# Optimization experiments

Measured on AMD Instinct MI355X. Metric: run time of the kernel, lower is better.

The kernel has to match this reference:

```python
import jax, jax.numpy as jnp
import numpy as np

B, L, D = 4, 2048, 1024

def setup_inputs() -> dict:
    key = jax.random.key(0)
    k = jax.random.split(key, 5)
    s = 1.0 / np.sqrt(D)
    return {
        "x": jax.random.normal(k[0], (B, L, D), dtype=jnp.float32),
        "W1": jax.random.uniform(k[1], (D, D), jnp.float32, -s, s),
        "b1": jax.random.uniform(k[2], (D,), jnp.float32, -s, s),
        "W2": jax.random.uniform(k[3], (D, D), jnp.float32, -s, s),
        "b2": jax.random.uniform(k[4], (D,), jnp.float32, -s, s),
    }

def reference(x, W1, b1, W2, b2):
    # query = fc1(x), value = fc2(x); torch Linear: x @ W^T + b
    query = jnp.einsum("bld,ed->ble", x, W1) + b1   # [B,L,D]
    value = jnp.einsum("bld,ed->ble", x, W2) + b2   # [B,L,D]
    # attn = softmax(query @ value^T)  (dot attention, no scaling in original)
    scores = jnp.einsum("bqd,bkd->bqk", query, value)  # [B,L,L]
    attn = jax.nn.softmax(scores, axis=-1)
    # dropout_p=0.0 -> identity
    return jnp.einsum("bqk,bkd->bqd", attn, value)     # [B,L,D]
```

## Files before the change

kernel.cpp:

```cpp
#include <hip/hip_runtime.h>
#include <stdint.h>
#include <stddef.h>


typedef _Float16  f16_t;
typedef _Float16  f16x8 __attribute__((ext_vector_type(8)));
typedef float     f32x4 __attribute__((ext_vector_type(4)));

__device__ __forceinline__ f32x4 mfma16(f16x8 a, f16x8 b, f32x4 c) {
  return __builtin_amdgcn_mfma_f32_16x16x32_f16(a, b, c, 0, 0, 0);
}

__device__ __forceinline__ void async_copy16(const f16_t* g, f16_t* l) {
  __builtin_amdgcn_global_load_lds(
      (const __attribute__((address_space(1))) unsigned int*)(g),
      (__attribute__((address_space(3))) unsigned int*)(l),
      16, 0, 0);
}

template <int RM, int RN, int NS>
__device__ __forceinline__ void gemm_core(
    const f16_t* __restrict__ A, const f16_t* __restrict__ B,
    int lda, int ldb, int nk,
    f16_t* __restrict__ As, f16_t* __restrict__ Bs, f32x4 (&acc)[RM][RN])
{
  const int tid  = threadIdx.x;
  const int lane = tid & 63;
  const int w    = tid >> 6;
  const int wr   = (w >> 1) * (RM * 16);
  const int wc   = (w & 1) * (RN * 16);
  const int l16  = lane & 15;
  const int quad = lane >> 4;
  const int sw   = (quad ^ ((l16 >> 1) & 3)) * 8;

  const int r0  = tid >> 2;
  const int kc0 = ((tid & 3) ^ ((r0 >> 1) & 3)) * 8;

  const f16_t* Ag = A + (size_t)r0 * lda + kc0;
  const f16_t* Bg = B + (size_t)r0 * ldb + kc0;

  for (int kt = 0; kt < nk; ++kt) {
#pragma unroll
    for (int s = 0; s < NS; ++s) {
      const int ko = s * 32;
#pragma unroll
      for (int h = 0; h < RM / 2; ++h)
        async_copy16(Ag + ko + (size_t)(64 * h) * lda,
                     As + s * RM * 1024 + (tid + 256 * h) * 8);
#pragma unroll
      for (int h = 0; h < RN / 2; ++h)
        async_copy16(Bg + ko + (size_t)(64 * h) * ldb,
                     Bs + s * RN * 1024 + (tid + 256 * h) * 8);
    }
    __syncthreads();

#pragma unroll
    for (int s = 0; s < NS; ++s) {
      const f16_t* Ac = As + s * RM * 1024;
      const f16_t* Bc = Bs + s * RN * 1024;
      f16x8 af[RM], bf[RN];
#pragma unroll
      for (int i = 0; i < RM; ++i)
        af[i] = *(const f16x8*)(Ac + (wr + i * 16 + l16) * 32 + sw);
#pragma unroll
      for (int j = 0; j < RN; ++j)
        bf[j] = *(const f16x8*)(Bc + (wc + j * 16 + l16) * 32 + sw);
#pragma unroll
      for (int i = 0; i < RM; ++i)
#pragma unroll
        for (int j = 0; j < RN; ++j)
          acc[i][j] = mfma16(af[i], bf[j], acc[i][j]);
    }

    __syncthreads();
    Ag += NS * 32; Bg += NS * 32;
  }
}

__global__ __launch_bounds__(256) void cvt_kernel(
    const float* __restrict__ x, const float* __restrict__ W1,
    const float* __restrict__ W2, f16_t* __restrict__ xh,
    f16_t* __restrict__ W1h, f16_t* __restrict__ W2h)
{
  const size_t XN = (size_t)8192 * 1024;
  const size_t WN = (size_t)1024 * 1024;
  size_t i = ((size_t)blockIdx.x * 256 + threadIdx.x) * 8;
  const float* in; f16_t* out;
  if (i < XN)            { in = x;  out = xh; }
  else if (i < XN + WN)  { in = W1; out = W1h; i -= XN; }
  else                   { in = W2; out = W2h; i -= XN + WN; }
  f32x4 a = *(const f32x4*)(in + i);
  f32x4 b = *(const f32x4*)(in + i + 4);
  f16x8 o;
#pragma unroll
  for (int k = 0; k < 4; ++k) { o[k] = (f16_t)a[k]; o[k + 4] = (f16_t)b[k]; }
  *(f16x8*)(out + i) = o;
}

__global__ __launch_bounds__(256) void proj_qv_kernel(
    const f16_t* __restrict__ X, const f16_t* __restrict__ W1,
    const f16_t* __restrict__ W2, const float* __restrict__ b1,
    const float* __restrict__ b2, f16_t* __restrict__ Q,
    f16_t* __restrict__ V)
{
  __shared__ __align__(16) f16_t Xs[2 * 64 * 32];
  __shared__ __align__(16) f16_t W1s[2 * 64 * 32];
  __shared__ __align__(16) f16_t W2s[2 * 64 * 32];
  constexpr int SZ = 64 * 32;

  const int m0 = blockIdx.x * 64;
  const int n0 = blockIdx.y * 64;

  const int tid  = threadIdx.x;
  const int lane = tid & 63;
  const int w    = tid >> 6;
  const int wr   = (w >> 1) * 32;
  const int wc   = (w & 1) * 32;
  const int quad = lane >> 4;
  const int l16  = lane & 15;
  const int sw   = (quad ^ ((l16 >> 1) & 3)) * 8;
  const int r0   = tid >> 2;
  const int kc0  = ((tid & 3) ^ ((r0 >> 1) & 3)) * 8;

  const f16_t* Xg = X + (size_t)(m0 + r0) * 1024 + kc0;
  const f16_t* G1 = W1 + (size_t)(n0 + r0) * 1024 + kc0;
  const f16_t* G2 = W2 + (size_t)(n0 + r0) * 1024 + kc0;

  f32x4 accQ[2][2] = {};
  f32x4 accV[2][2] = {};

  for (int kt = 0; kt < 16; ++kt) {
#pragma unroll
    for (int s = 0; s < 2; ++s) {
      const int ko = s * 32;
      async_copy16(Xg + ko, Xs + s * SZ + tid * 8);
      async_copy16(G1 + ko, W1s + s * SZ + tid * 8);
      async_copy16(G2 + ko, W2s + s * SZ + tid * 8);
    }
    __syncthreads();

#pragma unroll
    for (int s = 0; s < 2; ++s) {
      f16x8 xf[2], w1f[2], w2f[2];
#pragma unroll
      for (int i = 0; i < 2; ++i) {
        xf[i]  = *(const f16x8*)(Xs  + s * SZ + (wr + i * 16 + l16) * 32 + sw);
        w1f[i] = *(const f16x8*)(W1s + s * SZ + (wc + i * 16 + l16) * 32 + sw);
        w2f[i] = *(const f16x8*)(W2s + s * SZ + (wc + i * 16 + l16) * 32 + sw);
      }
#pragma unroll
      for (int i = 0; i < 2; ++i)
#pragma unroll
        for (int j = 0; j < 2; ++j) {
          accQ[i][j] = mfma16(xf[i], w1f[j], accQ[i][j]);
          accV[i][j] = mfma16(xf[i], w2f[j], accV[i][j]);
        }
    }
    __syncthreads();
    Xg += 64; G1 += 64; G2 += 64;
  }

#pragma unroll
  for (int j = 0; j < 2; ++j) {
    const int col = n0 + wc + j * 16 + l16;
    const float bq = b1[col], bv = b2[col];
#pragma unroll
    for (int i = 0; i < 2; ++i)
#pragma unroll
      for (int r = 0; r < 4; ++r) {
        const int row = m0 + wr + i * 16 + quad * 4 + r;
        Q[(size_t)row * 1024 + col] = (f16_t)(accQ[i][j][r] + bq);
        V[(size_t)row * 1024 + col] = (f16_t)(accV[i][j][r] + bv);
      }
  }
}

__global__ __launch_bounds__(256) void vt_kernel(
    const f16_t* __restrict__ V, f16_t* __restrict__ Vt)
{
  __shared__ __align__(16) f16_t Ls[64 * 64];
  const int key0 = blockIdx.x * 64;
  const int d0   = blockIdx.y * 64;
  const size_t boff = (size_t)blockIdx.z * 2048 * 1024;

  const int tid = threadIdx.x;
#pragma unroll
  for (int rep = 0; rep < 2; ++rep) {
    const int kr = rep * 32 + (tid >> 3);
    const int dc = (tid & 7) * 8;
    f16x8 v = *(const f16x8*)(V + boff + (size_t)(key0 + kr) * 1024 + d0 + dc);
#pragma unroll
    for (int e = 0; e < 8; ++e) {
      const int d = dc + e;
      Ls[d * 64 + (((kr >> 3) ^ (d >> 3)) << 3) + (kr & 7)] = v[e];
    }
  }
  __syncthreads();
#pragma unroll
  for (int rep = 0; rep < 2; ++rep) {
    const int d = rep * 32 + (tid >> 3);
    const int c = tid & 7;
    f16x8 v = *(const f16x8*)(Ls + d * 64 + ((c ^ (d >> 3)) << 3));
    *(f16x8*)(Vt + boff + (size_t)(d0 + d) * 2048 + key0 + c * 8) = v;
  }
}

__global__ __launch_bounds__(256) void score_kernel(
    const f16_t* __restrict__ Q, const f16_t* __restrict__ V,
    f16_t* __restrict__ S)
{
  __shared__ __align__(16) f16_t As[2 * 128 * 32];
  __shared__ __align__(16) f16_t Bs[2 * 128 * 32];
  const int m0 = blockIdx.x * 128;
  const int n0 = blockIdx.y * 128;
  const size_t boff = (size_t)blockIdx.z * 2048 * 1024;

  f32x4 acc[4][4] = {};
  gemm_core<4, 4, 2>(Q + boff + (size_t)m0 * 1024,
                     V + boff + (size_t)n0 * 1024,
                     1024, 1024, 1024 / 64, As, Bs, acc);

  f16_t* Sb = S + (size_t)blockIdx.z * 2048 * 2048;
  const int lane = threadIdx.x & 63;
  const int w    = threadIdx.x >> 6;
  const int wr   = (w >> 1) * 64, wc = (w & 1) * 64;
  const int quad = lane >> 4,     l16 = lane & 15;

#pragma unroll
  for (int i = 0; i < 4; ++i)
#pragma unroll
    for (int j = 0; j < 4; ++j)
#pragma unroll
      for (int r = 0; r < 4; ++r) {
        const int row = m0 + wr + i * 16 + quad * 4 + r;
        const int col = n0 + wc + j * 16 + l16;
        Sb[(size_t)row * 2048 + col] = (f16_t)acc[i][j][r];
      }
}

__global__ __launch_bounds__(256) void softmax_kernel(f16_t* __restrict__ S)
{
  f16_t* row = S + (size_t)blockIdx.x * 2048;
  const int tid  = threadIdx.x;
  const int lane = tid & 63;
  const int w    = tid >> 6;

  f16x8 v = *((const f16x8*)row + tid);
  float f[8];
#pragma unroll
  for (int k = 0; k < 8; ++k) f[k] = (float)v[k];

  float m = f[0];
#pragma unroll
  for (int k = 1; k < 8; ++k) m = fmaxf(m, f[k]);
#pragma unroll
  for (int off = 32; off >= 1; off >>= 1) m = fmaxf(m, __shfl_xor(m, off));

  __shared__ float red[4];
  if (lane == 0) red[w] = m;
  __syncthreads();
  m = fmaxf(fmaxf(red[0], red[1]), fmaxf(red[2], red[3]));

  float s = 0.f;
#pragma unroll
  for (int k = 0; k < 8; ++k) { f[k] = __expf(f[k] - m); s += f[k]; }
#pragma unroll
  for (int off = 32; off >= 1; off >>= 1) s += __shfl_xor(s, off);
  __syncthreads();
  if (lane == 0) red[w] = s;
  __syncthreads();
  s = (red[0] + red[1]) + (red[2] + red[3]);
  const float inv = 1.f / s;

  f16x8 o;
#pragma unroll
  for (int k = 0; k < 8; ++k) o[k] = (f16_t)(f[k] * inv);
  *((f16x8*)row + tid) = o;
}

__global__ __launch_bounds__(256) void out_kernel(
    const f16_t* __restrict__ P, const f16_t* __restrict__ Vt,
    float* __restrict__ Out)
{
  __shared__ __align__(16) f16_t As[4 * 64 * 32];
  __shared__ __align__(16) f16_t Bs[4 * 128 * 32];
  const int m0 = blockIdx.x * 64;
  const int n0 = blockIdx.y * 128;
  const size_t poff  = (size_t)blockIdx.z * 2048 * 2048;
  const size_t vtoff = (size_t)blockIdx.z * 1024 * 2048;

  f32x4 acc[2][4] = {};
  gemm_core<2, 4, 4>(P + poff + (size_t)m0 * 2048,
                     Vt + vtoff + (size_t)n0 * 2048,
                     2048, 2048, 2048 / 128, As, Bs, acc);

  float* Ob = Out + (size_t)blockIdx.z * 2048 * 1024;
  const int lane = threadIdx.x & 63;
  const int w    = threadIdx.x >> 6;
  const int wr   = (w >> 1) * 32, wc = (w & 1) * 64;
  const int quad = lane >> 4,     l16 = lane & 15;

#pragma unroll
  for (int i = 0; i < 2; ++i)
#pragma unroll
    for (int j = 0; j < 4; ++j)
#pragma unroll
      for (int r = 0; r < 4; ++r) {
        const int row = m0 + wr + i * 16 + quad * 4 + r;
        const int col = n0 + wc + j * 16 + l16;
        Ob[(size_t)row * 1024 + col] = acc[i][j][r];
      }
}

extern "C" void kernel_launch(void* const* d_in, const int* in_sizes, int n_in,
                              void* d_out, int out_size, void* d_ws, size_t ws_size,
                              hipStream_t stream) {
  const float* x  = (const float*)d_in[0];
  const float* W1 = (const float*)d_in[1];
  const float* b1 = (const float*)d_in[2];
  const float* W2 = (const float*)d_in[3];
  const float* b2 = (const float*)d_in[4];
  float* out = (float*)d_out;

  const size_t QN = (size_t)8192 * 1024;
  const size_t WN = (size_t)1024 * 1024;
  f16_t* xh  = (f16_t*)d_ws;
  f16_t* W1h = xh + QN;
  f16_t* W2h = W1h + WN;
  f16_t* Q   = W2h + WN;
  f16_t* V   = Q + QN;
  f16_t* Vt  = V + QN;
  f16_t* S   = Vt + QN;

  dim3 blk(256);
  cvt_kernel<<<5120, blk, 0, stream>>>(x, W1, W2, xh, W1h, W2h);
  proj_qv_kernel<<<dim3(128, 16), blk, 0, stream>>>(xh, W1h, W2h, b1, b2, Q, V);
  vt_kernel<<<dim3(32, 16, 4), blk, 0, stream>>>(V, Vt);
  score_kernel<<<dim3(16, 16, 4), blk, 0, stream>>>(Q, V, S);
  softmax_kernel<<<8192, blk, 0, stream>>>(S);
  out_kernel<<<dim3(32, 8, 4), blk, 0, stream>>>(S, Vt, out);
}
```

Measured before the change: 258.6 us.

## Fuse V transpose into projection epilogue and shrink out_kernel pipeline depth

The projection kernel now writes the transposed V tile through shared memory (reusing the W1 staging buffer) in its epilogue. This removes the separate vt_kernel launch and its re-read of V from global memory. Separately, out_kernel switches from 4 stages with a K-step of 128 to 2 stages with a K-step of 64, which cuts LDS use and may raise occupancy at the cost of less prefetch depth. Reusing W1s for the transpose depends on a barrier after the main loop, since other waves may still be reading that buffer.

```diff
diff --git a/kernel.cpp b/kernel.cpp
--- a/kernel.cpp
+++ b/kernel.cpp
@@ -101,7 +101,7 @@
     const f16_t* __restrict__ X, const f16_t* __restrict__ W1,
     const f16_t* __restrict__ W2, const float* __restrict__ b1,
     const float* __restrict__ b2, f16_t* __restrict__ Q,
-    f16_t* __restrict__ V)
+    f16_t* __restrict__ V, f16_t* __restrict__ Vt)
 {
   __shared__ __align__(16) f16_t Xs[2 * 64 * 32];
   __shared__ __align__(16) f16_t W1s[2 * 64 * 32];
@@ -160,48 +160,34 @@
     Xg += 64; G1 += 64; G2 += 64;
   }
 
+  f16_t* Ts = W1s;
 #pragma unroll
   for (int j = 0; j < 2; ++j) {
-    const int col = n0 + wc + j * 16 + l16;
+    const int c   = wc + j * 16 + l16;
+    const int col = n0 + c;
     const float bq = b1[col], bv = b2[col];
 #pragma unroll
     for (int i = 0; i < 2; ++i)
 #pragma unroll
       for (int r = 0; r < 4; ++r) {
-        const int row = m0 + wr + i * 16 + quad * 4 + r;
-        Q[(size_t)row * 1024 + col] = (f16_t)(accQ[i][j][r] + bq);
-        V[(size_t)row * 1024 + col] = (f16_t)(accV[i][j][r] + bv);
+        const int k   = wr + i * 16 + quad * 4 + r;
+        const int row = m0 + k;
+        const float q = accQ[i][j][r] + bq;
+        const float v = accV[i][j][r] + bv;
+        Q[(size_t)row * 1024 + col] = (f16_t)q;
+        V[(size_t)row * 1024 + col] = (f16_t)v;
+        Ts[c * 64 + (((k >> 3) ^ (c >> 3)) << 3) + (k & 7)] = (f16_t)v;
       }
   }
-}
-
-__global__ __launch_bounds__(256) void vt_kernel(
-    const f16_t* __restrict__ V, f16_t* __restrict__ Vt)
-{
-  __shared__ __align__(16) f16_t Ls[64 * 64];
-  const int key0 = blockIdx.x * 64;
-  const int d0   = blockIdx.y * 64;
-  const size_t boff = (size_t)blockIdx.z * 2048 * 1024;
-
-  const int tid = threadIdx.x;
-#pragma unroll
-  for (int rep = 0; rep < 2; ++rep) {
-    const int kr = rep * 32 + (tid >> 3);
-    const int dc = (tid & 7) * 8;
-    f16x8 v = *(const f16x8*)(V + boff + (size_t)(key0 + kr) * 1024 + d0 + dc);
-#pragma unroll
-    for (int e = 0; e < 8; ++e) {
-      const int d = dc + e;
-      Ls[d * 64 + (((kr >> 3) ^ (d >> 3)) << 3) + (kr & 7)] = v[e];
-    }
-  }
   __syncthreads();
+
+  const size_t vtbase = ((size_t)(m0 >> 11) << 21) + (size_t)n0 * 2048 + (m0 & 2047);
 #pragma unroll
   for (int rep = 0; rep < 2; ++rep) {
     const int d = rep * 32 + (tid >> 3);
     const int c = tid & 7;
-    f16x8 v = *(const f16x8*)(Ls + d * 64 + ((c ^ (d >> 3)) << 3));
-    *(f16x8*)(Vt + boff + (size_t)(d0 + d) * 2048 + key0 + c * 8) = v;
+    f16x8 vv = *(const f16x8*)(Ts + d * 64 + ((c ^ (d >> 3)) << 3));
+    *(f16x8*)(Vt + vtbase + (size_t)d * 2048 + c * 8) = vv;
   }
 }
 
@@ -282,17 +268,17 @@
     const f16_t* __restrict__ P, const f16_t* __restrict__ Vt,
     float* __restrict__ Out)
 {
-  __shared__ __align__(16) f16_t As[4 * 64 * 32];
-  __shared__ __align__(16) f16_t Bs[4 * 128 * 32];
+  __shared__ __align__(16) f16_t As[2 * 64 * 32];
+  __shared__ __align__(16) f16_t Bs[2 * 128 * 32];
   const int m0 = blockIdx.x * 64;
   const int n0 = blockIdx.y * 128;
   const size_t poff  = (size_t)blockIdx.z * 2048 * 2048;
   const size_t vtoff = (size_t)blockIdx.z * 1024 * 2048;
 
   f32x4 acc[2][4] = {};
-  gemm_core<2, 4, 4>(P + poff + (size_t)m0 * 2048,
+  gemm_core<2, 4, 2>(P + poff + (size_t)m0 * 2048,
                      Vt + vtoff + (size_t)n0 * 2048,
-                     2048, 2048, 2048 / 128, As, Bs, acc);
+                     2048, 2048, 2048 / 64, As, Bs, acc);
 
   float* Ob = Out + (size_t)blockIdx.z * 2048 * 1024;
   const int lane = threadIdx.x & 63;
@@ -334,8 +320,7 @@
 
   dim3 blk(256);
   cvt_kernel<<<5120, blk, 0, stream>>>(x, W1, W2, xh, W1h, W2h);
-  proj_qv_kernel<<<dim3(128, 16), blk, 0, stream>>>(xh, W1h, W2h, b1, b2, Q, V);
-  vt_kernel<<<dim3(32, 16, 4), blk, 0, stream>>>(V, Vt);
+  proj_qv_kernel<<<dim3(128, 16), blk, 0, stream>>>(xh, W1h, W2h, b1, b2, Q, V, Vt);
   score_kernel<<<dim3(16, 16, 4), blk, 0, stream>>>(Q, V, S);
   softmax_kernel<<<8192, blk, 0, stream>>>(S);
   out_kernel<<<dim3(32, 8, 4), blk, 0, stream>>>(S, Vt, out);
```

After: 249.8 us. 3.4% less time.
